# Kernel optimization log

Measured on AMD Instinct MI355X. Metric: run time of the kernel, lower is better.

The kernel has to match this reference:

```python
import jax, jax.numpy as jnp
import numpy as np

IN_FEATURES = 8192
OUT_FEATURES = 8192
MAX_STATES = 100
THRESHOLD = MAX_STATES // 2  # 50


def setup_inputs() -> dict:
    key = jax.random.key(0)
    k1, k2 = jax.random.split(key)
    spike_input = jax.random.uniform(k1, (IN_FEATURES,), dtype=jnp.float32)
    # buffer init: randn(out, in) * 2.0 + threshold - 1.0
    synapse_states = (jax.random.normal(k2, (OUT_FEATURES, IN_FEATURES), dtype=jnp.float32)
                      * 2.0 + float(THRESHOLD) - 1.0)
    membrane_potential = jnp.zeros((OUT_FEATURES,), dtype=jnp.float32)
    adaptive_threshold = jnp.full((OUT_FEATURES,), 2.5, dtype=jnp.float32)
    eligibility_trace = jnp.zeros((OUT_FEATURES, IN_FEATURES), dtype=jnp.float32)
    return {
        'spike_input': spike_input,
        'synapse_states': synapse_states,
        'membrane_potential': membrane_potential,
        'adaptive_threshold': adaptive_threshold,
        'eligibility_trace': eligibility_trace,
    }


def reference(spike_input, synapse_states, membrane_potential, adaptive_threshold, eligibility_trace):
    # ternary (here effectively binary) weights via threshold compare
    w = (synapse_states > float(THRESHOLD)).astype(jnp.float32)  # [O, I]
    x = spike_input.reshape(-1)                                   # [I] (batch must be 1)
    current = w @ x                                               # [O]
    # LIF membrane update: v <- 0.8*v + I
    v_mem = membrane_potential * 0.8 + current
    spikes = (v_mem >= adaptive_threshold).astype(jnp.float32)    # [O]
    # eligibility trace: decay + outer-product potentiation, clamp to [0, 10]
    new_trace = jnp.clip(eligibility_trace * 0.7 + jnp.outer(spikes, x) * 3.0, 0.0, 10.0)
    # adaptive threshold homeostasis, clamp to [0.5, 10]
    new_threshold = jnp.clip(adaptive_threshold + (spikes - 0.05) * 0.1, 0.5, 10.0)
    # soft reset: v <- v * (1 - spike) * 0.2
    new_v_mem = v_mem * (1.0 - spikes) * 0.2
    return spikes, new_v_mem, new_trace, new_threshold
```

## Files before the change

kernel.cpp:

```cpp
#include <hip/hip_runtime.h>

#define IN_F 8192
#define OUT_F 8192
#define BLOCK 256
#define WAVES_PER_BLOCK (BLOCK / 64)
#define N4 (IN_F / 4)

typedef float v4f __attribute__((ext_vector_type(4)));

__global__ __launch_bounds__(BLOCK) void snn_fused_kernel(
    const float* __restrict__ x,
    const float* __restrict__ syn,
    const float* __restrict__ mp,
    const float* __restrict__ at,
    const float* __restrict__ trace,
    float* __restrict__ spikes_out,
    float* __restrict__ vmem_out,
    float* __restrict__ trace_out,
    float* __restrict__ thr_out)
{
    const int wave = threadIdx.x >> 6;
    const int lane = threadIdx.x & 63;
    const int o    = blockIdx.x * WAVES_PER_BLOCK + wave;

    const v4f* __restrict__ syn4 = reinterpret_cast<const v4f*>(syn + (size_t)o * IN_F);
    const v4f* __restrict__ x4   = reinterpret_cast<const v4f*>(x);

    float partial = 0.0f;
    #pragma unroll 8
    for (int i = lane; i < N4; i += 64) {
        v4f s  = syn4[i];
        v4f xv = x4[i];
        partial += (s.x > 50.0f ? xv.x : 0.0f);
        partial += (s.y > 50.0f ? xv.y : 0.0f);
        partial += (s.z > 50.0f ? xv.z : 0.0f);
        partial += (s.w > 50.0f ? xv.w : 0.0f);
    }

    #pragma unroll
    for (int off = 32; off > 0; off >>= 1)
        partial += __shfl_down(partial, off, 64);
    const float cur = __shfl(partial, 0, 64);

    const float v  = mp[o] * 0.8f + cur;
    const float a  = at[o];
    const float sp = (v >= a) ? 1.0f : 0.0f;
    if (lane == 0) {
        spikes_out[o] = sp;
        vmem_out[o]   = v * (1.0f - sp) * 0.2f;
        thr_out[o]    = fminf(fmaxf(a + (sp - 0.05f) * 0.1f, 0.5f), 10.0f);
    }

    const float sp3 = sp * 3.0f;
    const v4f* __restrict__ tr4 = reinterpret_cast<const v4f*>(trace + (size_t)o * IN_F);
    v4f*       out4             = reinterpret_cast<v4f*>(trace_out + (size_t)o * IN_F);

    #pragma unroll 8
    for (int i = lane; i < N4; i += 64) {
        v4f t  = tr4[i];
        v4f xv = x4[i];
        v4f r;
        r.x = fminf(fmaxf(t.x * 0.7f + sp3 * xv.x, 0.0f), 10.0f);
        r.y = fminf(fmaxf(t.y * 0.7f + sp3 * xv.y, 0.0f), 10.0f);
        r.z = fminf(fmaxf(t.z * 0.7f + sp3 * xv.z, 0.0f), 10.0f);
        r.w = fminf(fmaxf(t.w * 0.7f + sp3 * xv.w, 0.0f), 10.0f);
        __builtin_nontemporal_store(r, &out4[i]);
    }
}

extern "C" void kernel_launch(void* const* d_in, const int* in_sizes, int n_in,
                              void* d_out, int out_size, void* d_ws, size_t ws_size,
                              hipStream_t stream) {
    const float* x     = (const float*)d_in[0];
    const float* syn   = (const float*)d_in[1];
    const float* mp    = (const float*)d_in[2];
    const float* at    = (const float*)d_in[3];
    const float* trace = (const float*)d_in[4];

    float* out        = (float*)d_out;
    float* spikes_out = out;
    float* vmem_out   = out + OUT_F;
    float* trace_out  = out + 2 * (size_t)OUT_F;
    float* thr_out    = out + 2 * (size_t)OUT_F + (size_t)OUT_F * IN_F;

    snn_fused_kernel<<<OUT_F / WAVES_PER_BLOCK, BLOCK, 0, stream>>>(
        x, syn, mp, at, trace, spikes_out, vmem_out, trace_out, thr_out);
}
```

Before: 157.1 us.

## Split fused SNN kernel into block-per-row GEMV and grid-stride trace update

Splits the fused kernel into two launches. The first computes each output row's dot product with a full 256-thread block and a shared-memory reduction. The second is a flat grid-stride elementwise kernel that updates the eligibility trace, reading spikes back from global memory and using ordinary stores instead of nontemporal ones. The goal is better parallelism and memory streaming for each phase, at the cost of an extra launch and giving up the overlap of the two phases that the fused kernel allowed.

```diff
diff --git a/kernel.cpp b/kernel.cpp
--- a/kernel.cpp
+++ b/kernel.cpp
@@ -2,33 +2,30 @@
 
 #define IN_F 8192
 #define OUT_F 8192
+#define N4 (IN_F / 4)
 #define BLOCK 256
-#define WAVES_PER_BLOCK (BLOCK / 64)
-#define N4 (IN_F / 4)
 
 typedef float v4f __attribute__((ext_vector_type(4)));
 
-__global__ __launch_bounds__(BLOCK) void snn_fused_kernel(
+__global__ __launch_bounds__(BLOCK) void snn_gemv_kernel(
     const float* __restrict__ x,
     const float* __restrict__ syn,
     const float* __restrict__ mp,
     const float* __restrict__ at,
-    const float* __restrict__ trace,
     float* __restrict__ spikes_out,
     float* __restrict__ vmem_out,
-    float* __restrict__ trace_out,
     float* __restrict__ thr_out)
 {
-    const int wave = threadIdx.x >> 6;
-    const int lane = threadIdx.x & 63;
-    const int o    = blockIdx.x * WAVES_PER_BLOCK + wave;
+    const int o   = blockIdx.x;
+    const int tid = threadIdx.x;
 
     const v4f* __restrict__ syn4 = reinterpret_cast<const v4f*>(syn + (size_t)o * IN_F);
     const v4f* __restrict__ x4   = reinterpret_cast<const v4f*>(x);
 
     float partial = 0.0f;
-    #pragma unroll 8
-    for (int i = lane; i < N4; i += 64) {
+    #pragma unroll
+    for (int k = 0; k < N4 / BLOCK; ++k) {
+        const int i = tid + k * BLOCK;
         v4f s  = syn4[i];
         v4f xv = x4[i];
         partial += (s.x > 50.0f ? xv.x : 0.0f);
@@ -40,31 +37,50 @@
     #pragma unroll
     for (int off = 32; off > 0; off >>= 1)
         partial += __shfl_down(partial, off, 64);
-    const float cur = __shfl(partial, 0, 64);
 
-    const float v  = mp[o] * 0.8f + cur;
-    const float a  = at[o];
-    const float sp = (v >= a) ? 1.0f : 0.0f;
-    if (lane == 0) {
+    __shared__ float wsum[BLOCK / 64];
+    if ((tid & 63) == 0) wsum[tid >> 6] = partial;
+    __syncthreads();
+
+    if (tid == 0) {
+        float cur = wsum[0] + wsum[1] + wsum[2] + wsum[3];
+        float v   = mp[o] * 0.8f + cur;
+        float a   = at[o];
+        float sp  = (v >= a) ? 1.0f : 0.0f;
         spikes_out[o] = sp;
         vmem_out[o]   = v * (1.0f - sp) * 0.2f;
         thr_out[o]    = fminf(fmaxf(a + (sp - 0.05f) * 0.1f, 0.5f), 10.0f);
     }
+}
 
-    const float sp3 = sp * 3.0f;
-    const v4f* __restrict__ tr4 = reinterpret_cast<const v4f*>(trace + (size_t)o * IN_F);
-    v4f*       out4             = reinterpret_cast<v4f*>(trace_out + (size_t)o * IN_F);
+#define B_GRID 2048
+#define B_THREADS ((size_t)B_GRID * BLOCK)
+#define B_ITERS ((size_t)OUT_F * N4 / B_THREADS)
+
+__global__ __launch_bounds__(BLOCK) void snn_trace_kernel(
+    const float* __restrict__ x,
+    const float* __restrict__ trace,
+    const float* __restrict__ spikes,
+    float* __restrict__ trace_out)
+{
+    const size_t g0 = (size_t)blockIdx.x * BLOCK + threadIdx.x;
+
+    const v4f* __restrict__ tr4 = reinterpret_cast<const v4f*>(trace);
+    const v4f* __restrict__ x4  = reinterpret_cast<const v4f*>(x);
+    v4f* __restrict__ out4      = reinterpret_cast<v4f*>(trace_out);
 
     #pragma unroll 8
-    for (int i = lane; i < N4; i += 64) {
-        v4f t  = tr4[i];
-        v4f xv = x4[i];
+    for (size_t k = 0; k < B_ITERS; ++k) {
+        const size_t g = g0 + k * B_THREADS;
+        v4f t   = tr4[g];
+        v4f xv  = x4[g & (N4 - 1)];
+        float s3 = spikes[g >> 11] * 3.0f;
         v4f r;
-        r.x = fminf(fmaxf(t.x * 0.7f + sp3 * xv.x, 0.0f), 10.0f);
-        r.y = fminf(fmaxf(t.y * 0.7f + sp3 * xv.y, 0.0f), 10.0f);
-        r.z = fminf(fmaxf(t.z * 0.7f + sp3 * xv.z, 0.0f), 10.0f);
-        r.w = fminf(fmaxf(t.w * 0.7f + sp3 * xv.w, 0.0f), 10.0f);
-        __builtin_nontemporal_store(r, &out4[i]);
+        r.x = fminf(fmaxf(t.x * 0.7f + s3 * xv.x, 0.0f), 10.0f);
+        r.y = fminf(fmaxf(t.y * 0.7f + s3 * xv.y, 0.0f), 10.0f);
+        r.z = fminf(fmaxf(t.z * 0.7f + s3 * xv.z, 0.0f), 10.0f);
+        r.w = fminf(fmaxf(t.w * 0.7f + s3 * xv.w, 0.0f), 10.0f);
+        out4[g] = r;
     }
 }
 
@@ -83,6 +99,9 @@
     float* trace_out  = out + 2 * (size_t)OUT_F;
     float* thr_out    = out + 2 * (size_t)OUT_F + (size_t)OUT_F * IN_F;
 
-    snn_fused_kernel<<<OUT_F / WAVES_PER_BLOCK, BLOCK, 0, stream>>>(
-        x, syn, mp, at, trace, spikes_out, vmem_out, trace_out, thr_out);
+    snn_gemv_kernel<<<OUT_F, BLOCK, 0, stream>>>(
+        x, syn, mp, at, spikes_out, vmem_out, thr_out);
+
+    snn_trace_kernel<<<B_GRID, BLOCK, 0, stream>>>(
+        x, trace, spikes_out, trace_out);
 }
```

New measurement: 171.4 us. 9.1% more time.
